# Performance work log

Measured on AMD Instinct MI355X. Metric: run time of the kernel, lower is better.

The kernel has to match this reference:

```python
import jax, jax.numpy as jnp
import numpy as np

B, S, D, H = 2, 2048, 1024, 16
HD = D // H  # 64
LN_EPS = 1e-5


def setup_inputs() -> dict:
    key = jax.random.key(0)
    ks = jax.random.split(key, 10)
    s = 0.02
    return {
        "x": jax.random.normal(ks[0], (B, S, D), jnp.float32),
        "cdr_bias": jax.random.normal(ks[1], (B, S), jnp.float32),
        "Wq": jax.random.normal(ks[2], (D, D), jnp.float32) * s,
        "bq": jnp.zeros((D,), jnp.float32),
        "Wk": jax.random.normal(ks[3], (D, D), jnp.float32) * s,
        "bk": jnp.zeros((D,), jnp.float32),
        "Wv": jax.random.normal(ks[4], (D, D), jnp.float32) * s,
        "bv": jnp.zeros((D,), jnp.float32),
        "Wo": jax.random.normal(ks[5], (D, D), jnp.float32) * s,
        "bo": jnp.zeros((D,), jnp.float32),
        "gamma": jnp.ones((D,), jnp.float32),
        "beta": jnp.zeros((D,), jnp.float32),
        "cdr_weight": jnp.asarray(1.0, jnp.float32),
    }


def _rotate_half(t):
    # interleaved rotate: [-x2_0, x1_0, -x2_1, x1_1, ...] matching torch stack+reshape
    t1 = t[..., ::2]
    t2 = t[..., 1::2]
    return jnp.stack((-t2, t1), axis=-1).reshape(t.shape)


def reference(x, cdr_bias, Wq, bq, Wk, bk, Wv, bv, Wo, bo, gamma, beta, cdr_weight):
    b, s, d = x.shape

    # RoPE tables (faithful to original: sin/cos concatenated, rotate_half interleaved)
    pos = jnp.arange(s, dtype=x.dtype)
    inv_freq = 1.0 / (10000.0 ** (jnp.arange(0, HD, 2, dtype=x.dtype) / HD))
    sinusoid = pos[:, None] * inv_freq[None, :]              # [S, HD/2]
    sin_pos = jnp.concatenate([jnp.sin(sinusoid)] * 2, -1)   # [S, HD]
    cos_pos = jnp.concatenate([jnp.cos(sinusoid)] * 2, -1)
    sin_pos = sin_pos[None, None]                            # [1,1,S,HD]
    cos_pos = cos_pos[None, None]

    def heads(t):
        return t.reshape(b, s, H, HD).transpose(0, 2, 1, 3)  # [B,H,S,HD]

    Q = heads(x @ Wq + bq)
    K = heads(x @ Wk + bk)
    V = heads(x @ Wv + bv)

    Q = Q * cos_pos + _rotate_half(Q) * sin_pos
    K = K * cos_pos + _rotate_half(K) * sin_pos

    scores = jnp.einsum("bhqd,bhkd->bhqk", Q, K) / jnp.sqrt(jnp.asarray(HD, x.dtype))
    scores = scores + cdr_bias[:, None, None, :] * cdr_weight  # additive key-side bias
    probs = jax.nn.softmax(scores, axis=-1)                    # dropout = identity (eval)

    attn = jnp.einsum("bhqk,bhkd->bhqd", probs, V)
    attn = attn.transpose(0, 2, 1, 3).reshape(b, s, d)
    out = attn @ Wo + bo

    res = x + out
    mu = jnp.mean(res, axis=-1, keepdims=True)
    var = jnp.mean(jnp.square(res - mu), axis=-1, keepdims=True)
    return (res - mu) / jnp.sqrt(var + LN_EPS) * gamma + beta
```

## Files before the change

### kernel.cpp

```cpp
#include <hip/hip_runtime.h>
#include <hip/hip_bf16.h>
#include <math.h>

#define BB 2
#define SS 2048
#define DD 1024
#define HH 16
#define HD 64
#define MM (BB*SS)
#define LN_EPS 1e-5f
#define KVB 64
#define LOG2E 1.44269504088896340736f

typedef unsigned short u16;
typedef __attribute__((ext_vector_type(8))) short short8;
typedef __attribute__((ext_vector_type(4))) float f32x4;
typedef __attribute__((ext_vector_type(4))) unsigned short u16x4;

__device__ __forceinline__ u16 f2bf(float f) {
    union { __hip_bfloat16 h; u16 u; } cv;
    cv.h = __float2bfloat16(f);
    return cv.u;
}

__device__ __forceinline__ float exp2_(float x) {
    float r;
    asm("v_exp_f32 %0, %1" : "=v"(r) : "v"(x));
    return r;
}

__device__ __forceinline__ void gload16(const void* g, void* l) {
    __builtin_amdgcn_global_load_lds(
        (const __attribute__((address_space(1))) void*)g,
        (__attribute__((address_space(3))) void*)l, 16, 0, 0);
}

__global__ __launch_bounds__(256) void k_prep(
        const float* __restrict__ x,
        const float* __restrict__ Wq, const float* __restrict__ Wk,
        const float* __restrict__ Wv, const float* __restrict__ Wo,
        const float* __restrict__ cdr_bias, const float* __restrict__ cw,
        u16* __restrict__ xb, u16* __restrict__ wqkvt, u16* __restrict__ wot,
        float* __restrict__ cosb, float* __restrict__ sinb, float* __restrict__ biasf) {
    __shared__ float t[32][33];
    int bz = blockIdx.x, tid = threadIdx.x;
    if (bz < 4096) {
        int i = bz * 256 + tid;
        float4 v = ((const float4*)x)[i];
        u16x4 o;
        o[0] = f2bf(v.x); o[1] = f2bf(v.y); o[2] = f2bf(v.z); o[3] = f2bf(v.w);
        ((u16x4*)xb)[i] = o;
    } else if (bz < 8192) {
        int zb = bz - 4096;
        int z = zb >> 10, rem = zb & 1023;
        int k0 = (rem & 31) * 32, n0 = (rem >> 5) * 32;
        const float* W = (z == 0) ? Wq : (z == 1) ? Wk : (z == 2) ? Wv : Wo;
        u16* dst = (z < 3) ? (wqkvt + (size_t)z * DD * DD) : wot;
        int tx = tid & 31, ty = tid >> 5;
        #pragma unroll
        for (int r = 0; r < 32; r += 8)
            t[ty + r][tx] = W[(size_t)(k0 + ty + r) * DD + n0 + tx];
        __syncthreads();
        #pragma unroll
        for (int r = 0; r < 32; r += 8)
            dst[(size_t)(n0 + ty + r) * DD + k0 + tx] = f2bf(t[tx][ty + r]);
    } else {
        int idx = (bz - 8192) * 256 + tid;
        if (idx < BB * SS) biasf[idx] = cdr_bias[idx] * cw[0] * LOG2E;
        int s = idx >> 6, j = idx & 63;
        double invf = pow(10000.0, -((double)(2 * (j & 31))) / 64.0);
        double ang = (double)s * invf;
        cosb[idx] = (float)cos(ang);
        sinb[idx] = (float)sin(ang);
    }
}

#define GEMM_PIPE32(A_PTR, B_PTR)                                              \
    f32x4 acc[4][4] = {};                                                      \
    _Pragma("unroll")                                                          \
    for (int i = 0; i < 2; i++) {                                              \
        int p = i * 256 + tid;                                                 \
        int row = p >> 2, c = p & 3;                                           \
        gload16(A_PTR + (size_t)(bm + row) * DD + ((c ^ (row & 3)) << 3), Alds + p * 8); \
        gload16(B_PTR + (size_t)(bn + row) * DD + ((c ^ (row & 3)) << 3), Blds + p * 8); \
    }                                                                          \
    asm volatile("s_waitcnt vmcnt(0)" ::: "memory");                           \
    __builtin_amdgcn_s_barrier();                                              \
    for (int kt = 0; kt < 32; kt++) {                                          \
        int cur = kt & 1;                                                      \
        const u16* Acur = Alds + cur * (128 * 32);                             \
        const u16* Bcur = Blds + cur * (128 * 32);                             \
        if (kt + 1 < 32) {                                                     \
            u16* Anxt = Alds + (cur ^ 1) * (128 * 32);                         \
            u16* Bnxt = Blds + (cur ^ 1) * (128 * 32);                         \
            _Pragma("unroll")                                                  \
            for (int i = 0; i < 2; i++) {                                      \
                int p = i * 256 + tid;                                         \
                int row = p >> 2, c = p & 3;                                   \
                gload16(A_PTR + (size_t)(bm + row) * DD + (kt + 1) * 32 + ((c ^ (row & 3)) << 3), Anxt + p * 8); \
                gload16(B_PTR + (size_t)(bn + row) * DD + (kt + 1) * 32 + ((c ^ (row & 3)) << 3), Bnxt + p * 8); \
            }                                                                  \
        }                                                                      \
        short8 a[4], b[4];                                                     \
        int rch = (lg ^ (lr & 3)) << 3;                                        \
        _Pragma("unroll")                                                      \
        for (int i = 0; i < 4; i++) {                                          \
            a[i] = *(const short8*)(Acur + (wm * 64 + i * 16 + lr) * 32 + rch); \
            b[i] = *(const short8*)(Bcur + (wn * 64 + i * 16 + lr) * 32 + rch); \
        }                                                                      \
        __builtin_amdgcn_s_setprio(1);                                         \
        _Pragma("unroll")                                                      \
        for (int i = 0; i < 4; i++)                                            \
            _Pragma("unroll")                                                  \
            for (int j = 0; j < 4; j++)                                        \
                acc[i][j] = __builtin_amdgcn_mfma_f32_16x16x32_bf16(a[i], b[j], acc[i][j], 0, 0, 0); \
        __builtin_amdgcn_s_setprio(0);                                         \
        asm volatile("s_waitcnt vmcnt(0)" ::: "memory");                       \
        __builtin_amdgcn_s_barrier();                                          \
    }

__global__ __launch_bounds__(256, 4) void k_gemm_qkv(
        const u16* __restrict__ xb, const u16* __restrict__ wqkvt,
        const float* __restrict__ bq, const float* __restrict__ bk, const float* __restrict__ bv,
        const float* __restrict__ cosb, const float* __restrict__ sinb,
        u16* __restrict__ q, u16* __restrict__ k, u16* __restrict__ vt) {
    __shared__ u16 SMEM[17408];
    u16* Alds = SMEM;
    u16* Blds = SMEM + 8192;
    int tid = threadIdx.x;
    int lane = tid & 63, wid = tid >> 6;
    int wm = wid >> 1, wn = wid & 1;
    int bm = blockIdx.x * 128, bn = blockIdx.y * 128;
    int lr = lane & 15, lg = lane >> 4;

    GEMM_PIPE32(xb, wqkvt)

    int w = bn >> 10;
    if (w == 2) {
        u16* Tr = SMEM;
        #pragma unroll
        for (int j = 0; j < 4; j++) {
            int n_l = wn * 64 + j * 16 + lr;
            float bias = bv[(bn - 2048) + n_l];
            #pragma unroll
            for (int i = 0; i < 4; i++) {
                ushort4 pk;
                pk.x = f2bf(acc[i][j][0] + bias);
                pk.y = f2bf(acc[i][j][1] + bias);
                pk.z = f2bf(acc[i][j][2] + bias);
                pk.w = f2bf(acc[i][j][3] + bias);
                *(ushort4*)&Tr[n_l * 136 + wm * 64 + i * 16 + lg * 4] = pk;
            }
        }
        __syncthreads();
        int n_r = tid >> 1, hf = tid & 1;
        int nglob = (bn - 2048) + n_r;
        int b_ = bm >> 11;
        size_t vbase = ((size_t)(b_ * HH + (nglob >> 6)) * HD + (nglob & 63)) * SS
                     + (bm & 2047) + hf * 64;
        #pragma unroll
        for (int ii = 0; ii < 8; ii++)
            *(short8*)(vt + vbase + ii * 8) = *(const short8*)&Tr[n_r * 136 + hf * 64 + ii * 8];
    } else {
        int m0 = bm + wm * 64, n0 = bn + wn * 64;
        #pragma unroll
        for (int j = 0; j < 4; j++) {
            int n = n0 + j * 16 + lr;
            int n1 = n & 1023;
            int h = n1 >> 6, d = n1 & 63;
            float bias = (w == 0) ? bq[n1] : bk[n1];
            #pragma unroll
            for (int i = 0; i < 4; i++) {
                #pragma unroll
                for (int r = 0; r < 4; r++) {
                    int m = m0 + i * 16 + lg * 4 + r;
                    int b_ = m >> 11, s = m & 2047;
                    float val = acc[i][j][r] + bias;
                    float part = __shfl_xor(val, 1);
                    float c = cosb[s * 64 + d], sn = sinb[s * 64 + d];
                    float rot = (d & 1) ? part : -part;
                    val = val * c + rot * sn;
                    size_t bh = (size_t)(b_ * HH + h);
                    if (w == 0)
                        q[(bh * SS + s) * HD + d] = f2bf(val * (0.125f * LOG2E));
                    else
                        k[(bh * SS + s) * HD + d] = f2bf(val);
                }
            }
        }
    }
}

__global__ __launch_bounds__(256, 4) void k_gemm_o(
        const u16* __restrict__ attnb, const u16* __restrict__ wot,
        const float* __restrict__ bo, const float* __restrict__ x,
        float* __restrict__ res) {
    __shared__ u16 SMEM[16384];
    u16* Alds = SMEM;
    u16* Blds = SMEM + 8192;
    int tid = threadIdx.x;
    int lane = tid & 63, wid = tid >> 6;
    int wm = wid >> 1, wn = wid & 1;
    int bm = blockIdx.x * 128, bn = blockIdx.y * 128;
    int lr = lane & 15, lg = lane >> 4;

    GEMM_PIPE32(attnb, wot)

    int m0 = bm + wm * 64, n0 = bn + wn * 64;
    #pragma unroll
    for (int i = 0; i < 4; i++) {
        #pragma unroll
        for (int j = 0; j < 4; j++) {
            int n = n0 + j * 16 + lr;
            #pragma unroll
            for (int r = 0; r < 4; r++) {
                int m = m0 + i * 16 + lg * 4 + r;
                res[(size_t)m * DD + n] = acc[i][j][r] + bo[n] + x[(size_t)m * DD + n];
            }
        }
    }
}

__device__ __forceinline__ void stage64x64(const u16* __restrict__ gbase, size_t rstride,
                                           u16* lds, int tid) {
    int row = tid >> 3, c = tid & 7;
    gload16(gbase + (size_t)row * rstride + (size_t)((c ^ (row & 7)) << 3), lds + tid * 8);
}

__global__ __launch_bounds__(512, 4) void k_attn(
        const u16* __restrict__ q, const u16* __restrict__ kkv, const u16* __restrict__ vt,
        const float* __restrict__ biasf, u16* __restrict__ attnb) {
    __shared__ u16 Klds[2][64 * 64];
    __shared__ u16 Vlds[2][64 * 64];
    __shared__ u16 plds[8][16][72];

    int tid = threadIdx.x;
    int lane = tid & 63, wid = tid >> 6;
    int flat = blockIdx.y * gridDim.x + blockIdx.x;
    int bh = (flat & 7) * 4 + (flat >> 7);
    int qb = (flat >> 3) & 15;
    int b_ = bh >> 4, h = bh & 15;
    int q0 = qb * 128 + wid * 16;
    int lr = lane & 15, lg = lane >> 4;

    short8 qa[2];
    #pragma unroll
    for (int ks = 0; ks < 2; ks++)
        qa[ks] = *(const short8*)(q + ((size_t)bh * SS + q0 + lr) * HD + ks * 32 + lg * 8);

    stage64x64(kkv + ((size_t)bh * SS) * HD, HD, Klds[0], tid);
    stage64x64(vt + ((size_t)bh * HD) * SS, SS, Vlds[0], tid);
    __syncthreads();

    f32x4 acco[4] = {};
    f32x4 acS = {};
    const float* bias_b = biasf + (size_t)b_ * SS;
    short8 vone;
    #pragma unroll
    for (int j = 0; j < 8; j++) vone[j] = (short)0x3F80;

    for (int t = 0; t < SS / KVB; t++) {
        int cur = t & 1;
        if (t + 1 < SS / KVB) {
            int kv1 = (t + 1) * KVB;
            stage64x64(kkv + ((size_t)bh * SS + kv1) * HD, HD, Klds[cur ^ 1], tid);
            stage64x64(vt + ((size_t)bh * HD) * SS + kv1, SS, Vlds[cur ^ 1], tid);
        }
        const u16* Kc = Klds[cur];
        const u16* Vc = Vlds[cur];

        f32x4 s_[4];
        #pragma unroll
        for (int n = 0; n < 4; n++) {
            float4 b4 = *(const float4*)(bias_b + t * KVB + n * 16 + lg * 4);
            s_[n][0] = b4.x; s_[n][1] = b4.y; s_[n][2] = b4.z; s_[n][3] = b4.w;
        }

        short8 kf[4][2], vf[4][2];
        #pragma unroll
        for (int n = 0; n < 4; n++) {
            int row = n * 16 + lr;
            #pragma unroll
            for (int ks = 0; ks < 2; ks++)
                kf[n][ks] = *(const short8*)(Kc + row * 64 + (((ks * 4 + lg) ^ (lr & 7)) << 3));
        }
        #pragma unroll
        for (int dt = 0; dt < 4; dt++) {
            int row = dt * 16 + lr;
            #pragma unroll
            for (int kt = 0; kt < 2; kt++)
                vf[dt][kt] = *(const short8*)(Vc + row * 64 + (((kt * 4 + lg) ^ (lr & 7)) << 3));
        }

        __builtin_amdgcn_s_setprio(1);
        #pragma unroll
        for (int n = 0; n < 4; n++) {
            s_[n] = __builtin_amdgcn_mfma_f32_16x16x32_bf16(kf[n][0], qa[0], s_[n], 0, 0, 0);
            s_[n] = __builtin_amdgcn_mfma_f32_16x16x32_bf16(kf[n][1], qa[1], s_[n], 0, 0, 0);
        }
        __builtin_amdgcn_s_setprio(0);

        #pragma unroll
        for (int n = 0; n < 4; n++) {
            ushort4 pk;
            pk.x = f2bf(exp2_(s_[n][0]));
            pk.y = f2bf(exp2_(s_[n][1]));
            pk.z = f2bf(exp2_(s_[n][2]));
            pk.w = f2bf(exp2_(s_[n][3]));
            *(ushort4*)&plds[wid][lr][n * 16 + lg * 4] = pk;
        }
        asm volatile("s_waitcnt lgkmcnt(0)" ::: "memory");
        __builtin_amdgcn_s_setprio(1);
        #pragma unroll
        for (int kt = 0; kt < 2; kt++) {
            short8 pa = *(const short8*)&plds[wid][lr][kt * 32 + lg * 8];
            #pragma unroll
            for (int dt = 0; dt < 4; dt++)
                acco[dt] = __builtin_amdgcn_mfma_f32_16x16x32_bf16(pa, vf[dt][kt], acco[dt], 0, 0, 0);
            acS = __builtin_amdgcn_mfma_f32_16x16x32_bf16(pa, vone, acS, 0, 0, 0);
        }
        __builtin_amdgcn_s_setprio(0);
        __syncthreads();
    }

    float linv[4];
    #pragma unroll
    for (int r = 0; r < 4; r++) linv[r] = 1.f / acS[r];
    #pragma unroll
    for (int dt = 0; dt < 4; dt++)
        #pragma unroll
        for (int r = 0; r < 4; r++)
            attnb[((size_t)b_ * SS + q0 + lg * 4 + r) * DD + h * HD + dt * 16 + lr] =
                f2bf(acco[dt][r] * linv[r]);
}

__global__ __launch_bounds__(256) void k_ln(const float* __restrict__ res,
        const float* __restrict__ gamma, const float* __restrict__ beta,
        float* __restrict__ out) {
    int row = blockIdx.x, tid = threadIdx.x;
    float4 v = ((const float4*)(res + (size_t)row * DD))[tid];
    float s = v.x + v.y + v.z + v.w;
    float ss = v.x * v.x + v.y * v.y + v.z * v.z + v.w * v.w;
    #pragma unroll
    for (int off = 32; off; off >>= 1) { s += __shfl_xor(s, off); ss += __shfl_xor(ss, off); }
    __shared__ float sbuf[8];
    int wid = tid >> 6, lane = tid & 63;
    if (lane == 0) { sbuf[wid] = s; sbuf[4 + wid] = ss; }
    __syncthreads();
    s = sbuf[0] + sbuf[1] + sbuf[2] + sbuf[3];
    ss = sbuf[4] + sbuf[5] + sbuf[6] + sbuf[7];
    float mu = s * (1.f / DD);
    float var = ss * (1.f / DD) - mu * mu;
    float rstd = rsqrtf(var + LN_EPS);
    float4 g = ((const float4*)gamma)[tid];
    float4 be = ((const float4*)beta)[tid];
    float4 o;
    o.x = (v.x - mu) * rstd * g.x + be.x;
    o.y = (v.y - mu) * rstd * g.y + be.y;
    o.z = (v.z - mu) * rstd * g.z + be.z;
    o.w = (v.w - mu) * rstd * g.w + be.w;
    ((float4*)(out + (size_t)row * DD))[tid] = o;
}

extern "C" void kernel_launch(void* const* d_in, const int* in_sizes, int n_in,
                              void* d_out, int out_size, void* d_ws, size_t ws_size,
                              hipStream_t stream) {
    const float* x        = (const float*)d_in[0];
    const float* cdr_bias = (const float*)d_in[1];
    const float* Wq       = (const float*)d_in[2];
    const float* bq       = (const float*)d_in[3];
    const float* Wk       = (const float*)d_in[4];
    const float* bk       = (const float*)d_in[5];
    const float* Wv       = (const float*)d_in[6];
    const float* bv       = (const float*)d_in[7];
    const float* Wo       = (const float*)d_in[8];
    const float* bo       = (const float*)d_in[9];
    const float* gamma    = (const float*)d_in[10];
    const float* beta     = (const float*)d_in[11];
    const float* cw       = (const float*)d_in[12];

    char* ws = (char*)d_ws;
    const size_t MB = 1048576;
    u16*   xb     = (u16*)(ws + 0);
    u16*   wqkvt  = (u16*)(ws + 8 * MB);
    u16*   wot    = (u16*)(ws + 14 * MB);
    u16*   qb     = (u16*)(ws + 16 * MB);
    u16*   kb     = (u16*)(ws + 24 * MB);
    u16*   vtb    = (u16*)(ws + 32 * MB);
    u16*   attnb  = (u16*)(ws + 40 * MB);
    float* res    = (float*)(ws + 48 * MB);
    float* biasf  = (float*)(ws + 48 * MB);
    float* cosb   = (float*)(ws + 64 * MB);
    float* sinb   = (float*)(ws + 64 * MB + 524288);

    k_prep     <<<8704, 256, 0, stream>>>(x, Wq, Wk, Wv, Wo, cdr_bias, cw,
                                          xb, wqkvt, wot, cosb, sinb, biasf);
    k_gemm_qkv <<<dim3(32, 24), 256, 0, stream>>>(xb, wqkvt, bq, bk, bv, cosb, sinb, qb, kb, vtb);
    k_attn     <<<dim3(16, 32), 512, 0, stream>>>(qb, kb, vtb, biasf, attnb);
    k_gemm_o   <<<dim3(32, 8), 256, 0, stream>>>(attnb, wot, bo, x, res);
    k_ln       <<<4096, 256, 0, stream>>>(res, gamma, beta, (float*)d_out);
}
```

Measured before the change: 133.4 us.

## Use 32x32x16 MFMA in attention with register-resident probabilities and 4-wave blocks

Rewrites the attention kernel so each of 4 waves handles 32 query rows using 32x32x16 bf16 MFMAs instead of 8 waves with 16x16x32. Probabilities are passed to the PV MFMA through cross-lane shuffles instead of a per-wave LDS round trip. The row sum is accumulated in scalar registers plus a final shuffle, replacing the extra ones-vector MFMA. This cuts LDS traffic and MFMA instruction count per tile. In exchange it raises register pressure and halves the waves per block, which may reduce latency hiding.

```diff
diff --git a/kernel.cpp b/kernel.cpp
--- a/kernel.cpp
+++ b/kernel.cpp
@@ -13,14 +13,20 @@
 #define LOG2E 1.44269504088896340736f
 
 typedef unsigned short u16;
+typedef unsigned int u32;
 typedef __attribute__((ext_vector_type(8))) short short8;
 typedef __attribute__((ext_vector_type(4))) float f32x4;
+typedef __attribute__((ext_vector_type(16))) float f32x16;
 typedef __attribute__((ext_vector_type(4))) unsigned short u16x4;
+typedef __attribute__((ext_vector_type(4))) unsigned int u32x4;
 
 __device__ __forceinline__ u16 f2bf(float f) {
     union { __hip_bfloat16 h; u16 u; } cv;
     cv.h = __float2bfloat16(f);
     return cv.u;
+}
+__device__ __forceinline__ u32 pk2(float a, float b) {
+    return (u32)f2bf(a) | ((u32)f2bf(b) << 16);
 }
 
 __device__ __forceinline__ float exp2_(float x) {
@@ -221,117 +227,130 @@
     }
 }
 
-__device__ __forceinline__ void stage64x64(const u16* __restrict__ gbase, size_t rstride,
-                                           u16* lds, int tid) {
-    int row = tid >> 3, c = tid & 7;
-    gload16(gbase + (size_t)row * rstride + (size_t)((c ^ (row & 7)) << 3), lds + tid * 8);
-}
-
-__global__ __launch_bounds__(512, 4) void k_attn(
+__device__ __forceinline__ void stage64x64_256(const u16* __restrict__ gbase, size_t rstride,
+                                               u16* lds, int tid) {
+    #pragma unroll
+    for (int i = 0; i < 2; i++) {
+        int L = i * 256 + tid;
+        int row = L >> 3, c = L & 7;
+        gload16(gbase + (size_t)row * rstride + (size_t)((c ^ (row & 7)) << 3), lds + L * 8);
+    }
+}
+
+__global__ __launch_bounds__(256, 2) void k_attn(
         const u16* __restrict__ q, const u16* __restrict__ kkv, const u16* __restrict__ vt,
         const float* __restrict__ biasf, u16* __restrict__ attnb) {
     __shared__ u16 Klds[2][64 * 64];
     __shared__ u16 Vlds[2][64 * 64];
-    __shared__ u16 plds[8][16][72];
 
     int tid = threadIdx.x;
     int lane = tid & 63, wid = tid >> 6;
+    int l31 = lane & 31, hi = lane >> 5;
     int flat = blockIdx.y * gridDim.x + blockIdx.x;
     int bh = (flat & 7) * 4 + (flat >> 7);
     int qb = (flat >> 3) & 15;
     int b_ = bh >> 4, h = bh & 15;
-    int q0 = qb * 128 + wid * 16;
-    int lr = lane & 15, lg = lane >> 4;
-
-    short8 qa[2];
+    int q0 = qb * 128 + wid * 32;
+
+    short8 qa[4];
     #pragma unroll
-    for (int ks = 0; ks < 2; ks++)
-        qa[ks] = *(const short8*)(q + ((size_t)bh * SS + q0 + lr) * HD + ks * 32 + lg * 8);
-
-    stage64x64(kkv + ((size_t)bh * SS) * HD, HD, Klds[0], tid);
-    stage64x64(vt + ((size_t)bh * HD) * SS, SS, Vlds[0], tid);
+    for (int dk = 0; dk < 4; dk++)
+        qa[dk] = *(const short8*)(q + ((size_t)bh * SS + q0 + l31) * HD + dk * 16 + hi * 8);
+
+    stage64x64_256(kkv + ((size_t)bh * SS) * HD, HD, Klds[0], tid);
+    stage64x64_256(vt + ((size_t)bh * HD) * SS, SS, Vlds[0], tid);
     __syncthreads();
 
-    f32x4 acco[4] = {};
-    f32x4 acS = {};
+    f32x16 acco[2] = {};
+    float rs = 0.f;
     const float* bias_b = biasf + (size_t)b_ * SS;
-    short8 vone;
-    #pragma unroll
-    for (int j = 0; j < 8; j++) vone[j] = (short)0x3F80;
 
     for (int t = 0; t < SS / KVB; t++) {
         int cur = t & 1;
         if (t + 1 < SS / KVB) {
             int kv1 = (t + 1) * KVB;
-            stage64x64(kkv + ((size_t)bh * SS + kv1) * HD, HD, Klds[cur ^ 1], tid);
-            stage64x64(vt + ((size_t)bh * HD) * SS + kv1, SS, Vlds[cur ^ 1], tid);
+            stage64x64_256(kkv + ((size_t)bh * SS + kv1) * HD, HD, Klds[cur ^ 1], tid);
+            stage64x64_256(vt + ((size_t)bh * HD) * SS + kv1, SS, Vlds[cur ^ 1], tid);
         }
         const u16* Kc = Klds[cur];
         const u16* Vc = Vlds[cur];
 
-        f32x4 s_[4];
-        #pragma unroll
-        for (int n = 0; n < 4; n++) {
-            float4 b4 = *(const float4*)(bias_b + t * KVB + n * 16 + lg * 4);
-            s_[n][0] = b4.x; s_[n][1] = b4.y; s_[n][2] = b4.z; s_[n][3] = b4.w;
-        }
-
-        short8 kf[4][2], vf[4][2];
-        #pragma unroll
-        for (int n = 0; n < 4; n++) {
-            int row = n * 16 + lr;
-            #pragma unroll
-            for (int ks = 0; ks < 2; ks++)
-                kf[n][ks] = *(const short8*)(Kc + row * 64 + (((ks * 4 + lg) ^ (lr & 7)) << 3));
-        }
-        #pragma unroll
-        for (int dt = 0; dt < 4; dt++) {
-            int row = dt * 16 + lr;
-            #pragma unroll
-            for (int kt = 0; kt < 2; kt++)
-                vf[dt][kt] = *(const short8*)(Vc + row * 64 + (((kt * 4 + lg) ^ (lr & 7)) << 3));
-        }
-
+        short8 kf[2][4], vf[2][4];
+        #pragma unroll
+        for (int n = 0; n < 2; n++) {
+            int row = n * 32 + l31;
+            #pragma unroll
+            for (int dk = 0; dk < 4; dk++)
+                kf[n][dk] = *(const short8*)(Kc + row * 64 + ((((dk << 1) + hi) ^ (row & 7)) << 3));
+        }
+        #pragma unroll
+        for (int dt = 0; dt < 2; dt++) {
+            int row = dt * 32 + l31;
+            #pragma unroll
+            for (int m = 0; m < 4; m++)
+                vf[dt][m] = *(const short8*)(Vc + row * 64 + ((((m << 1) + hi) ^ (row & 7)) << 3));
+        }
+
+        f32x16 s_[2];
+        #pragma unroll
+        for (int n = 0; n < 2; n++)
+            #pragma unroll
+            for (int g = 0; g < 4; g++) {
+                float4 b4 = *(const float4*)(bias_b + t * KVB + n * 32 + g * 8 + hi * 4);
+                s_[n][g * 4 + 0] = b4.x; s_[n][g * 4 + 1] = b4.y;
+                s_[n][g * 4 + 2] = b4.z; s_[n][g * 4 + 3] = b4.w;
+            }
         __builtin_amdgcn_s_setprio(1);
         #pragma unroll
-        for (int n = 0; n < 4; n++) {
-            s_[n] = __builtin_amdgcn_mfma_f32_16x16x32_bf16(kf[n][0], qa[0], s_[n], 0, 0, 0);
-            s_[n] = __builtin_amdgcn_mfma_f32_16x16x32_bf16(kf[n][1], qa[1], s_[n], 0, 0, 0);
-        }
+        for (int n = 0; n < 2; n++)
+            #pragma unroll
+            for (int dk = 0; dk < 4; dk++)
+                s_[n] = __builtin_amdgcn_mfma_f32_32x32x16_bf16(kf[n][dk], qa[dk], s_[n], 0, 0, 0);
         __builtin_amdgcn_s_setprio(0);
 
         #pragma unroll
-        for (int n = 0; n < 4; n++) {
-            ushort4 pk;
-            pk.x = f2bf(exp2_(s_[n][0]));
-            pk.y = f2bf(exp2_(s_[n][1]));
-            pk.z = f2bf(exp2_(s_[n][2]));
-            pk.w = f2bf(exp2_(s_[n][3]));
-            *(ushort4*)&plds[wid][lr][n * 16 + lg * 4] = pk;
-        }
-        asm volatile("s_waitcnt lgkmcnt(0)" ::: "memory");
-        __builtin_amdgcn_s_setprio(1);
-        #pragma unroll
-        for (int kt = 0; kt < 2; kt++) {
-            short8 pa = *(const short8*)&plds[wid][lr][kt * 32 + lg * 8];
-            #pragma unroll
-            for (int dt = 0; dt < 4; dt++)
-                acco[dt] = __builtin_amdgcn_mfma_f32_16x16x32_bf16(pa, vf[dt][kt], acco[dt], 0, 0, 0);
-            acS = __builtin_amdgcn_mfma_f32_16x16x32_bf16(pa, vone, acS, 0, 0, 0);
-        }
-        __builtin_amdgcn_s_setprio(0);
+        for (int n = 0; n < 2; n++) {
+            float p[16];
+            #pragma unroll
+            for (int r = 0; r < 16; r++) {
+                p[r] = exp2_(s_[n][r]);
+                rs += p[r];
+            }
+            #pragma unroll
+            for (int w2 = 0; w2 < 2; w2++) {
+                int base = w2 * 8;
+                u32 ua = pk2(p[base + 0], p[base + 1]);
+                u32 ub = pk2(p[base + 2], p[base + 3]);
+                u32 uc = pk2(p[base + 4], p[base + 5]);
+                u32 ud = pk2(p[base + 6], p[base + 7]);
+                u32 ta = __shfl_xor(ua, 32), tb = __shfl_xor(ub, 32);
+                u32 tc = __shfl_xor(uc, 32), td = __shfl_xor(ud, 32);
+                u32x4 paw;
+                paw[0] = hi ? tc : ua;
+                paw[1] = hi ? td : ub;
+                paw[2] = hi ? uc : ta;
+                paw[3] = hi ? ud : tb;
+                short8 pa;
+                __builtin_memcpy(&pa, &paw, 16);
+                __builtin_amdgcn_s_setprio(1);
+                acco[0] = __builtin_amdgcn_mfma_f32_32x32x16_bf16(pa, vf[0][2 * n + w2], acco[0], 0, 0, 0);
+                acco[1] = __builtin_amdgcn_mfma_f32_32x32x16_bf16(pa, vf[1][2 * n + w2], acco[1], 0, 0, 0);
+                __builtin_amdgcn_s_setprio(0);
+            }
+        }
         __syncthreads();
     }
 
-    float linv[4];
+    rs += __shfl_xor(rs, 32);
+    float linv = 1.f / rs;
     #pragma unroll
-    for (int r = 0; r < 4; r++) linv[r] = 1.f / acS[r];
-    #pragma unroll
-    for (int dt = 0; dt < 4; dt++)
-        #pragma unroll
-        for (int r = 0; r < 4; r++)
-            attnb[((size_t)b_ * SS + q0 + lg * 4 + r) * DD + h * HD + dt * 16 + lr] =
-                f2bf(acco[dt][r] * linv[r]);
+    for (int r = 0; r < 16; r++) {
+        int qr = (r & 3) + 8 * (r >> 2) + 4 * hi;
+        float lv = __shfl(linv, qr);
+        size_t orow = ((size_t)b_ * SS + q0 + qr) * DD + h * HD + l31;
+        attnb[orow]      = f2bf(acco[0][r] * lv);
+        attnb[orow + 32] = f2bf(acco[1][r] * lv);
+    }
 }
 
 __global__ __launch_bounds__(256) void k_ln(const float* __restrict__ res,
@@ -396,7 +415,7 @@
     k_prep     <<<8704, 256, 0, stream>>>(x, Wq, Wk, Wv, Wo, cdr_bias, cw,
                                           xb, wqkvt, wot, cosb, sinb, biasf);
     k_gemm_qkv <<<dim3(32, 24), 256, 0, stream>>>(xb, wqkvt, bq, bk, bv, cosb, sinb, qb, kb, vtb);
-    k_attn     <<<dim3(16, 32), 512, 0, stream>>>(qb, kb, vtb, biasf, attnb);
+    k_attn     <<<dim3(16, 32), 256, 0, stream>>>(qb, kb, vtb, biasf, attnb);
     k_gemm_o   <<<dim3(32, 8), 256, 0, stream>>>(attnb, wot, bo, x, res);
     k_ln       <<<4096, 256, 0, stream>>>(res, gamma, beta, (float*)d_out);
 }
```

New measurement: 145.9 us. 1.09x slower.

## Switch GEMM K-loop to triple-buffered LDS pipeline with partial vmcnt waits

Applied to the files above, without the earlier changes.

Replaces the double-buffered GEMM mainloop with a three-stage LDS ring. Tiles kt+1 and kt+2 are in flight while tile kt is computed, and each iteration waits only on older loads via vmcnt(4) with a single barrier instead of two waits per iteration. The goal is to hide more global-load latency and cut barrier stalls in the QKV and output projections. In exchange, LDS per block grows to 48 KB and launch bounds drop to 3 blocks per CU, which may reduce occupancy.

```diff
diff --git a/kernel.cpp b/kernel.cpp
--- a/kernel.cpp
+++ b/kernel.cpp
@@ -75,32 +75,29 @@
     }
 }
 
-#define GEMM_PIPE32(A_PTR, B_PTR)                                              \
+#define STAGE_T(A_PTR, B_PTR, T)                                               \
+    {                                                                          \
+        u16* Ab = Alds + ((T) % 3) * 4096;                                     \
+        u16* Bb = Blds + ((T) % 3) * 4096;                                     \
+        _Pragma("unroll")                                                      \
+        for (int i_ = 0; i_ < 2; i_++) {                                       \
+            int p_ = i_ * 256 + tid;                                           \
+            int row_ = p_ >> 2, c_ = p_ & 3;                                   \
+            gload16(A_PTR + (size_t)(bm + row_) * DD + (T) * 32 + ((c_ ^ (row_ & 3)) << 3), Ab + p_ * 8); \
+            gload16(B_PTR + (size_t)(bn + row_) * DD + (T) * 32 + ((c_ ^ (row_ & 3)) << 3), Bb + p_ * 8); \
+        }                                                                      \
+    }
+
+#define GEMM_PIPE3(A_PTR, B_PTR)                                               \
     f32x4 acc[4][4] = {};                                                      \
-    _Pragma("unroll")                                                          \
-    for (int i = 0; i < 2; i++) {                                              \
-        int p = i * 256 + tid;                                                 \
-        int row = p >> 2, c = p & 3;                                           \
-        gload16(A_PTR + (size_t)(bm + row) * DD + ((c ^ (row & 3)) << 3), Alds + p * 8); \
-        gload16(B_PTR + (size_t)(bn + row) * DD + ((c ^ (row & 3)) << 3), Blds + p * 8); \
-    }                                                                          \
-    asm volatile("s_waitcnt vmcnt(0)" ::: "memory");                           \
-    __builtin_amdgcn_s_barrier();                                              \
+    STAGE_T(A_PTR, B_PTR, 0)                                                   \
+    STAGE_T(A_PTR, B_PTR, 1)                                                   \
     for (int kt = 0; kt < 32; kt++) {                                          \
-        int cur = kt & 1;                                                      \
-        const u16* Acur = Alds + cur * (128 * 32);                             \
-        const u16* Bcur = Blds + cur * (128 * 32);                             \
-        if (kt + 1 < 32) {                                                     \
-            u16* Anxt = Alds + (cur ^ 1) * (128 * 32);                         \
-            u16* Bnxt = Blds + (cur ^ 1) * (128 * 32);                         \
-            _Pragma("unroll")                                                  \
-            for (int i = 0; i < 2; i++) {                                      \
-                int p = i * 256 + tid;                                         \
-                int row = p >> 2, c = p & 3;                                   \
-                gload16(A_PTR + (size_t)(bm + row) * DD + (kt + 1) * 32 + ((c ^ (row & 3)) << 3), Anxt + p * 8); \
-                gload16(B_PTR + (size_t)(bn + row) * DD + (kt + 1) * 32 + ((c ^ (row & 3)) << 3), Bnxt + p * 8); \
-            }                                                                  \
-        }                                                                      \
+        if (kt < 31) asm volatile("s_waitcnt vmcnt(4)" ::: "memory");          \
+        else         asm volatile("s_waitcnt vmcnt(0)" ::: "memory");          \
+        __builtin_amdgcn_s_barrier();                                          \
+        const u16* Acur = Alds + (kt % 3) * 4096;                              \
+        const u16* Bcur = Blds + (kt % 3) * 4096;                              \
         short8 a[4], b[4];                                                     \
         int rch = (lg ^ (lr & 3)) << 3;                                        \
         _Pragma("unroll")                                                      \
@@ -108,6 +105,7 @@
             a[i] = *(const short8*)(Acur + (wm * 64 + i * 16 + lr) * 32 + rch); \
             b[i] = *(const short8*)(Bcur + (wn * 64 + i * 16 + lr) * 32 + rch); \
         }                                                                      \
+        if (kt + 2 < 32) STAGE_T(A_PTR, B_PTR, kt + 2)                         \
         __builtin_amdgcn_s_setprio(1);                                         \
         _Pragma("unroll")                                                      \
         for (int i = 0; i < 4; i++)                                            \
@@ -115,25 +113,24 @@
             for (int j = 0; j < 4; j++)                                        \
                 acc[i][j] = __builtin_amdgcn_mfma_f32_16x16x32_bf16(a[i], b[j], acc[i][j], 0, 0, 0); \
         __builtin_amdgcn_s_setprio(0);                                         \
-        asm volatile("s_waitcnt vmcnt(0)" ::: "memory");                       \
-        __builtin_amdgcn_s_barrier();                                          \
-    }
-
-__global__ __launch_bounds__(256, 4) void k_gemm_qkv(
+    }                                                                          \
+    __syncthreads();
+
+__global__ __launch_bounds__(256, 3) void k_gemm_qkv(
         const u16* __restrict__ xb, const u16* __restrict__ wqkvt,
         const float* __restrict__ bq, const float* __restrict__ bk, const float* __restrict__ bv,
         const float* __restrict__ cosb, const float* __restrict__ sinb,
         u16* __restrict__ q, u16* __restrict__ k, u16* __restrict__ vt) {
-    __shared__ u16 SMEM[17408];
+    __shared__ u16 SMEM[24576];
     u16* Alds = SMEM;
-    u16* Blds = SMEM + 8192;
+    u16* Blds = SMEM + 12288;
     int tid = threadIdx.x;
     int lane = tid & 63, wid = tid >> 6;
     int wm = wid >> 1, wn = wid & 1;
     int bm = blockIdx.x * 128, bn = blockIdx.y * 128;
     int lr = lane & 15, lg = lane >> 4;
 
-    GEMM_PIPE32(xb, wqkvt)
+    GEMM_PIPE3(xb, wqkvt)
 
     int w = bn >> 10;
     if (w == 2) {
@@ -191,20 +188,20 @@
     }
 }
 
-__global__ __launch_bounds__(256, 4) void k_gemm_o(
+__global__ __launch_bounds__(256, 3) void k_gemm_o(
         const u16* __restrict__ attnb, const u16* __restrict__ wot,
         const float* __restrict__ bo, const float* __restrict__ x,
         float* __restrict__ res) {
-    __shared__ u16 SMEM[16384];
+    __shared__ u16 SMEM[24576];
     u16* Alds = SMEM;
-    u16* Blds = SMEM + 8192;
+    u16* Blds = SMEM + 12288;
     int tid = threadIdx.x;
     int lane = tid & 63, wid = tid >> 6;
     int wm = wid >> 1, wn = wid & 1;
     int bm = blockIdx.x * 128, bn = blockIdx.y * 128;
     int lr = lane & 15, lg = lane >> 4;
 
-    GEMM_PIPE32(attnb, wot)
+    GEMM_PIPE3(attnb, wot)
 
     int m0 = bm + wm * 64, n0 = bn + wn * 64;
     #pragma unroll
```

Measured after the change: 123.7 us. 1.08x faster.
